# Kernel optimization log

Measured on AMD Instinct MI355X. Metric: run time of the kernel, lower is better.

The kernel has to match this reference:

```python
import jax, jax.numpy as jnp
import numpy as np

N = 50000      # total nodes (50 graphs x 1000 nodes)
G = 50         # number of graphs in the batch
NODE = 1000    # nodes per graph
E = 320000     # total edges (within-graph)
IN = 128
H1, H2 = 64, 128
HEADS = 4
NEG = 0.2      # LeakyReLU negative slope


def setup_inputs() -> dict:
    key = jax.random.key(0)
    ks = jax.random.split(key, 16)
    x = jax.random.normal(ks[0], (N, IN), jnp.float32)
    # edges confined to their own graph: per-graph offsets
    off = (jnp.arange(E) // (E // G)) * NODE
    src = jax.random.randint(ks[1], (E,), 0, NODE) + off
    dst = jax.random.randint(ks[2], (E,), 0, NODE) + off
    node2graph = jnp.arange(N) // NODE

    def lin(k, fan_in, fan_out):
        s = 1.0 / np.sqrt(fan_in)
        kw, kb = jax.random.split(k)
        return (jax.random.uniform(kw, (fan_in, fan_out), jnp.float32, -s, s),
                jax.random.uniform(kb, (fan_out,), jnp.float32, -s, s))

    W_src1, b_src1 = lin(ks[3], IN, HEADS * H1)
    W_dst1, b_dst1 = lin(ks[4], IN, HEADS * H1)
    attn1 = jax.random.normal(ks[5], (HEADS, H1), jnp.float32) * (1.0 / np.sqrt(H1))
    W_src2, b_src2 = lin(ks[6], H1, HEADS * H2)
    W_dst2, b_dst2 = lin(ks[7], H1, HEADS * H2)
    attn2 = jax.random.normal(ks[8], (HEADS, H2), jnp.float32) * (1.0 / np.sqrt(H2))
    gate_w, gate_b = lin(ks[9], H2, 1)
    return dict(x=x, src=src, dst=dst, node2graph=node2graph,
                W_src1=W_src1, b_src1=b_src1, W_dst1=W_dst1, b_dst1=b_dst1, attn1=attn1,
                W_src2=W_src2, b_src2=b_src2, W_dst2=W_dst2, b_dst2=b_dst2, attn2=attn2,
                gate_w=gate_w, gate_b=gate_b)


def gatv2_layer(h, src, dst, W_src, b_src, W_dst, b_dst, attn):
    # DGL GATv2Conv: e_ij = a^T LeakyReLU(W_src h_j + W_dst h_i), edge softmax over dst
    H, D = attn.shape
    fs = (h @ W_src + b_src).reshape(-1, H, D)  # [N,H,D]
    fd = (h @ W_dst + b_dst).reshape(-1, H, D)
    e = jax.nn.leaky_relu(fs[src] + fd[dst], NEG)        # [E,H,D]
    logits = jnp.einsum('ehd,hd->eh', e, attn)           # [E,H]
    m = jax.ops.segment_max(logits, dst, num_segments=h.shape[0])
    ex = jnp.exp(logits - m[dst])
    denom = jax.ops.segment_sum(ex, dst, num_segments=h.shape[0])
    alpha = ex / denom[dst]                              # [E,H]
    out = jax.ops.segment_sum(alpha[:, :, None] * fs[src], dst,
                              num_segments=h.shape[0])   # [N,H,D]
    return out


def reference(x, src, dst, node2graph,
              W_src1, b_src1, W_dst1, b_dst1, attn1,
              W_src2, b_src2, W_dst2, b_dst2, attn2,
              gate_w, gate_b):
    # layer 1 + head-wise maxpool -> [N, H1]
    h = gatv2_layer(x, src, dst, W_src1, b_src1, W_dst1, b_dst1, attn1).max(axis=1)
    # layer 2 + head-wise maxpool -> [N, H2]
    h = gatv2_layer(h, src, dst, W_src2, b_src2, W_dst2, b_dst2, attn2).max(axis=1)
    # global attention pooling: softmax(gate) over nodes per graph, weighted sum
    gate = h @ gate_w + gate_b                           # [N,1]
    gm = jax.ops.segment_max(gate, node2graph, num_segments=G)
    ge = jnp.exp(gate - gm[node2graph])
    gs = jax.ops.segment_sum(ge, node2graph, num_segments=G)
    alpha = ge / gs[node2graph]                          # [N,1]
    return jax.ops.segment_sum(alpha * h, node2graph, num_segments=G)  # [G, H2]
```

## Files before the change

kernel.cpp:

```cpp
#include <hip/hip_runtime.h>
#include <math.h>

#define NN 50000
#define GG 50
#define NODE 1000
#define EE 320000
#define HEADS 4

typedef __attribute__((ext_vector_type(8))) short short8;
typedef __attribute__((ext_vector_type(8))) __bf16 bf16x8;
typedef __attribute__((ext_vector_type(4))) float f32x4;

__device__ __forceinline__ unsigned short f2bf(float f) {
    unsigned int u = __float_as_uint(f);
    u = (u + 0x7fffu + ((u >> 16) & 1u)) >> 16;
    return (unsigned short)u;
}
__device__ __forceinline__ float bf2f(unsigned short s) {
    return __uint_as_float(((unsigned int)s) << 16);
}

__global__ void prep_cvt(const float* __restrict__ x, unsigned short* __restrict__ x_bf,
                         const float* __restrict__ W_src1, const float* __restrict__ W_dst1,
                         unsigned short* __restrict__ Wt1s, unsigned short* __restrict__ Wt1d,
                         const float* __restrict__ W_src2, const float* __restrict__ W_dst2,
                         unsigned short* __restrict__ Wt2s, unsigned short* __restrict__ Wt2d) {
    int i = blockIdx.x * 256 + threadIdx.x;
    int n4 = NN * 128 / 4;
    if (i < n4) {
        float4 f = *(const float4*)(x + (size_t)i * 4);
        ushort4 o;
        o.x = f2bf(f.x); o.y = f2bf(f.y); o.z = f2bf(f.z); o.w = f2bf(f.w);
        *(ushort4*)(x_bf + (size_t)i * 4) = o;
    }
    if (i < 256 * 128) {
        int n = i >> 7, k = i & 127;
        Wt1s[i] = f2bf(W_src1[k * 256 + n]);
        Wt1d[i] = f2bf(W_dst1[k * 256 + n]);
    }
    if (i < 512 * 64) {
        int n = i >> 6, k = i & 63;
        Wt2s[i] = f2bf(W_src2[k * 512 + n]);
        Wt2d[i] = f2bf(W_dst2[k * 512 + n]);
    }
}

__global__ void count_deg(const int* __restrict__ dst, int* __restrict__ deg, int E_) {
    int i = blockIdx.x * 256 + threadIdx.x;
    if (i < E_) atomicAdd(&deg[dst[i]], 1);
}

__global__ void scan1(const int* __restrict__ deg, int* __restrict__ bsum, int Nn) {
    __shared__ int sh[256];
    int i = blockIdx.x * 256 + threadIdx.x;
    sh[threadIdx.x] = (i < Nn) ? deg[i] : 0;
    __syncthreads();
    for (int s = 128; s > 0; s >>= 1) {
        if (threadIdx.x < s) sh[threadIdx.x] += sh[threadIdx.x + s];
        __syncthreads();
    }
    if (threadIdx.x == 0) bsum[blockIdx.x] = sh[0];
}

__global__ void scan3(const int* __restrict__ deg, const int* __restrict__ bsum,
                      int* __restrict__ rowptr, int* __restrict__ cursor, int Nn, int E_) {
    __shared__ int pr[256];
    __shared__ int sh[256];
    int bid = blockIdx.x;
    int pre = 0;
    for (int j = threadIdx.x; j < bid; j += 256) pre += bsum[j];
    pr[threadIdx.x] = pre;
    __syncthreads();
    for (int s = 128; s > 0; s >>= 1) {
        if (threadIdx.x < s) pr[threadIdx.x] += pr[threadIdx.x + s];
        __syncthreads();
    }
    int base = pr[0];
    __syncthreads();
    int i = bid * 256 + threadIdx.x;
    int v = (i < Nn) ? deg[i] : 0;
    sh[threadIdx.x] = v;
    __syncthreads();
    for (int s = 1; s < 256; s <<= 1) {
        int t = (threadIdx.x >= s) ? sh[threadIdx.x - s] : 0;
        __syncthreads();
        sh[threadIdx.x] += t;
        __syncthreads();
    }
    if (i < Nn) {
        int ex = sh[threadIdx.x] - v + base;
        rowptr[i] = ex;
        cursor[i] = ex;
    }
    if (bid == 0 && threadIdx.x == 0) rowptr[Nn] = E_;
}

__global__ void scatter_edges(const int* __restrict__ src, const int* __restrict__ dst,
                              int* __restrict__ cursor, int* __restrict__ csrc, int E_) {
    int i = blockIdx.x * 256 + threadIdx.x;
    if (i < E_) { int pos = atomicAdd(&cursor[dst[i]], 1); csrc[pos] = src[i]; }
}

template<int K>
__global__ __launch_bounds__(256)
void gemm_mfma(const unsigned short* __restrict__ A, const unsigned short* __restrict__ Wt,
               const float* __restrict__ bias, unsigned short* __restrict__ C,
               int M, int Ncols) {
    constexpr int BK = 64;
    __shared__ short A_lds[128 * BK];
    __shared__ short B_lds[128 * BK];
    constexpr int CH = BK / 8;
    constexpr int ROWB = BK * 2;
    int tid = threadIdx.x;
    int lane = tid & 63, wave = tid >> 6;
    int row0 = blockIdx.y * 128, col0 = blockIdx.x * 128;
    int wr = wave >> 1, wc = wave & 1;
    f32x4 acc[4][4] = {};

    for (int k0 = 0; k0 < K; k0 += BK) {
        if (k0) __syncthreads();
        for (int c = tid; c < 128 * CH; c += 256) {
            int r = c / CH, kc = c - r * CH;
            int gr = row0 + r; if (gr >= M) gr = M - 1;
            short8 v = *(const short8*)(A + (size_t)gr * K + k0 + kc * 8);
            *(short8*)((char*)A_lds + r * ROWB + ((kc * 16) ^ ((r & 7) << 4))) = v;
        }
        for (int c = tid; c < 128 * CH; c += 256) {
            int r = c / CH, kc = c - r * CH;
            short8 v = *(const short8*)(Wt + (size_t)(col0 + r) * K + k0 + kc * 8);
            *(short8*)((char*)B_lds + r * ROWB + ((kc * 16) ^ ((r & 7) << 4))) = v;
        }
        __syncthreads();

        #pragma unroll
        for (int ks = 0; ks < BK / 32; ++ks) {
            int kbyte = ks * 64 + ((lane >> 4) << 4);
            short8 a[4], b[4];
            #pragma unroll
            for (int m = 0; m < 4; ++m) {
                int r = wr * 64 + m * 16 + (lane & 15);
                a[m] = *(const short8*)((const char*)A_lds + r * ROWB + (kbyte ^ ((r & 7) << 4)));
            }
            #pragma unroll
            for (int n = 0; n < 4; ++n) {
                int r = wc * 64 + n * 16 + (lane & 15);
                b[n] = *(const short8*)((const char*)B_lds + r * ROWB + (kbyte ^ ((r & 7) << 4)));
            }
            #pragma unroll
            for (int m = 0; m < 4; ++m)
                #pragma unroll
                for (int n = 0; n < 4; ++n)
                    acc[m][n] = __builtin_amdgcn_mfma_f32_16x16x32_bf16(
                        __builtin_bit_cast(bf16x8, a[m]), __builtin_bit_cast(bf16x8, b[n]),
                        acc[m][n], 0, 0, 0);
        }
    }

    #pragma unroll
    for (int m = 0; m < 4; ++m) {
        int grb = row0 + wr * 64 + m * 16 + ((lane >> 4) << 2);
        #pragma unroll
        for (int q = 0; q < 4; ++q) {
            int gr = grb + q;
            if (gr < M) {
                #pragma unroll
                for (int n = 0; n < 4; ++n) {
                    int gc = col0 + wc * 64 + n * 16 + (lane & 15);
                    C[(size_t)gr * Ncols + gc] = f2bf(acc[m][n][q] + bias[gc]);
                }
            }
        }
    }
}

template<int D>
__global__ void gat_fused(const int* __restrict__ rowptr, const int* __restrict__ csrc,
                          const unsigned short* __restrict__ fs, const unsigned short* __restrict__ fd,
                          const float* __restrict__ attn, void* __restrict__ hout, int Nn) {
    int lane = threadIdx.x & 63;
    int wave = (blockIdx.x * blockDim.x + threadIdx.x) >> 6;
    int nw = (gridDim.x * blockDim.x) >> 6;
    constexpr int VE = D / 16;
    constexpr int HD = HEADS * D;
    int head = lane >> 4;
    int doff = (lane & 15) * VE;

    float at[VE];
    #pragma unroll
    for (int j = 0; j < VE; ++j) at[j] = attn[head * D + doff + j];

    for (int n = wave; n < Nn; n += nw) {
        int b = rowptr[n], e_ = rowptr[n + 1];
        float r[VE];
        if (b == e_) {
            #pragma unroll
            for (int k = 0; k < VE; ++k) r[k] = 0.f;
        } else {
            float fdf[VE];
            if constexpr (VE == 4) {
                ushort4 vd = *(const ushort4*)(fd + (size_t)n * HD + lane * 4);
                fdf[0] = bf2f(vd.x); fdf[1] = bf2f(vd.y); fdf[2] = bf2f(vd.z); fdf[3] = bf2f(vd.w);
            } else {
                short8 vd = *(const short8*)(fd + (size_t)n * HD + lane * 8);
                #pragma unroll
                for (int k = 0; k < 8; ++k) fdf[k] = bf2f((unsigned short)vd[k]);
            }
            float m = -INFINITY, l = 0.f;
            float acc[VE];
            #pragma unroll
            for (int k = 0; k < VE; ++k) acc[k] = 0.f;

            for (int j = b; j < e_; ++j) {
                int s = csrc[j];
                float fsf[VE];
                if constexpr (VE == 4) {
                    ushort4 vs = *(const ushort4*)(fs + (size_t)s * HD + lane * 4);
                    fsf[0] = bf2f(vs.x); fsf[1] = bf2f(vs.y); fsf[2] = bf2f(vs.z); fsf[3] = bf2f(vs.w);
                } else {
                    short8 vs = *(const short8*)(fs + (size_t)s * HD + lane * 8);
                    #pragma unroll
                    for (int k = 0; k < 8; ++k) fsf[k] = bf2f((unsigned short)vs[k]);
                }
                float p = 0.f;
                #pragma unroll
                for (int k = 0; k < VE; ++k) {
                    float v = fsf[k] + fdf[k];
                    v = v >= 0.f ? v : 0.2f * v;
                    p += v * at[k];
                }
                p += __shfl_xor(p, 1);
                p += __shfl_xor(p, 2);
                p += __shfl_xor(p, 4);
                p += __shfl_xor(p, 8);
                float mn = fmaxf(m, p);
                float sc = __expf(m - mn);
                float pw = __expf(p - mn);
                l = l * sc + pw;
                #pragma unroll
                for (int k = 0; k < VE; ++k) acc[k] = acc[k] * sc + pw * fsf[k];
                m = mn;
            }
            float inv = 1.f / l;
            #pragma unroll
            for (int k = 0; k < VE; ++k) r[k] = acc[k] * inv;
        }
        #pragma unroll
        for (int k = 0; k < VE; ++k) {
            r[k] = fmaxf(r[k], __shfl_xor(r[k], 16));
            r[k] = fmaxf(r[k], __shfl_xor(r[k], 32));
        }
        if (lane < 16) {
            if constexpr (VE == 4) {
                ushort4 o;
                o.x = f2bf(r[0]); o.y = f2bf(r[1]); o.z = f2bf(r[2]); o.w = f2bf(r[3]);
                *(ushort4*)((unsigned short*)hout + (size_t)n * 64 + doff) = o;
            } else {
                float* hp = (float*)hout + (size_t)n * 128 + doff;
                *(float4*)hp = make_float4(r[0], r[1], r[2], r[3]);
                *(float4*)(hp + 4) = make_float4(r[4], r[5], r[6], r[7]);
            }
        }
    }
}

__global__ void pool_kernel(const float* __restrict__ h2, const float* __restrict__ gate_w,
                            const float* __restrict__ gate_b, float* __restrict__ out) {
    __shared__ float gate[NODE];
    __shared__ float red[256];
    int g = blockIdx.x;
    int tid = threadIdx.x;
    const float* hb = h2 + (size_t)g * NODE * 128;
    float gb = gate_b[0];
    for (int n = tid; n < NODE; n += 256) {
        const float* r = hb + (size_t)n * 128;
        float acc = 0.f;
        #pragma unroll 8
        for (int k = 0; k < 128; ++k) acc += r[k] * gate_w[k];
        gate[n] = acc + gb;
    }
    __syncthreads();
    float m = -INFINITY;
    for (int n = tid; n < NODE; n += 256) m = fmaxf(m, gate[n]);
    red[tid] = m;
    __syncthreads();
    for (int s = 128; s > 0; s >>= 1) {
        if (tid < s) red[tid] = fmaxf(red[tid], red[tid + s]);
        __syncthreads();
    }
    m = red[0];
    __syncthreads();
    float ssum = 0.f;
    for (int n = tid; n < NODE; n += 256) {
        float e = __expf(gate[n] - m);
        gate[n] = e;
        ssum += e;
    }
    red[tid] = ssum;
    __syncthreads();
    for (int s = 128; s > 0; s >>= 1) {
        if (tid < s) red[tid] += red[tid + s];
        __syncthreads();
    }
    float inv = 1.f / red[0];
    __syncthreads();
    float acc = 0.f;
    int half = tid >> 7;
    int k = tid & 127;
    for (int n = half * 500; n < half * 500 + 500; ++n) acc += gate[n] * hb[(size_t)n * 128 + k];
    red[tid] = acc;
    __syncthreads();
    if (tid < 128) out[g * 128 + tid] = (red[tid] + red[tid + 128]) * inv;
}

extern "C" void kernel_launch(void* const* d_in, const int* in_sizes, int n_in,
                              void* d_out, int out_size, void* d_ws, size_t ws_size,
                              hipStream_t stream) {
    const float* x      = (const float*)d_in[0];
    const int*   src    = (const int*)d_in[1];
    const int*   dst    = (const int*)d_in[2];
    const float* W_src1 = (const float*)d_in[4];
    const float* b_src1 = (const float*)d_in[5];
    const float* W_dst1 = (const float*)d_in[6];
    const float* b_dst1 = (const float*)d_in[7];
    const float* attn1  = (const float*)d_in[8];
    const float* W_src2 = (const float*)d_in[9];
    const float* b_src2 = (const float*)d_in[10];
    const float* W_dst2 = (const float*)d_in[11];
    const float* b_dst2 = (const float*)d_in[12];
    const float* attn2  = (const float*)d_in[13];
    const float* gate_w = (const float*)d_in[14];
    const float* gate_b = (const float*)d_in[15];
    float* out = (float*)d_out;

    char* p = (char*)d_ws;
    auto alloc = [&](size_t bytes) -> void* {
        void* r = (void*)p;
        p += (bytes + 255) & ~(size_t)255;
        return r;
    };
    unsigned short* fs     = (unsigned short*)alloc((size_t)NN * 512 * 2);
    unsigned short* fd     = (unsigned short*)alloc((size_t)NN * 512 * 2);
    unsigned short* h1     = (unsigned short*)alloc((size_t)NN * 64 * 2);
    float*          h2     = (float*)alloc((size_t)NN * 128 * 4);
    unsigned short* x_bf   = (unsigned short*)alloc((size_t)NN * 128 * 2);
    unsigned short* Wt1s   = (unsigned short*)alloc((size_t)128 * 256 * 2);
    unsigned short* Wt1d   = (unsigned short*)alloc((size_t)128 * 256 * 2);
    unsigned short* Wt2s   = (unsigned short*)alloc((size_t)64 * 512 * 2);
    unsigned short* Wt2d   = (unsigned short*)alloc((size_t)64 * 512 * 2);
    int*            deg    = (int*)alloc((size_t)NN * 4);
    int*            rowptr = (int*)alloc((size_t)(NN + 1) * 4);
    int*            cursor = (int*)alloc((size_t)NN * 4);
    int*            csrc   = (int*)alloc((size_t)EE * 4);
    int*            bsum   = (int*)alloc(4096);

    prep_cvt<<<(NN * 128 / 4 + 255) / 256, 256, 0, stream>>>(
        x, x_bf, W_src1, W_dst1, Wt1s, Wt1d, W_src2, W_dst2, Wt2s, Wt2d);

    hipMemsetAsync(deg, 0, (size_t)NN * 4, stream);
    count_deg<<<(EE + 255) / 256, 256, 0, stream>>>(dst, deg, EE);
    int nb = (NN + 255) / 256;
    scan1<<<nb, 256, 0, stream>>>(deg, bsum, NN);
    scan3<<<nb, 256, 0, stream>>>(deg, bsum, rowptr, cursor, NN, EE);
    scatter_edges<<<(EE + 255) / 256, 256, 0, stream>>>(src, dst, cursor, csrc, EE);

    int rowtiles = (NN + 127) / 128;

    gemm_mfma<128><<<dim3(2, rowtiles), 256, 0, stream>>>(x_bf, Wt1s, b_src1, fs, NN, 256);
    gemm_mfma<128><<<dim3(2, rowtiles), 256, 0, stream>>>(x_bf, Wt1d, b_dst1, fd, NN, 256);
    gat_fused<64><<<2048, 256, 0, stream>>>(rowptr, csrc, fs, fd, attn1, h1, NN);

    gemm_mfma<64><<<dim3(4, rowtiles), 256, 0, stream>>>(h1, Wt2s, b_src2, fs, NN, 512);
    gemm_mfma<64><<<dim3(4, rowtiles), 256, 0, stream>>>(h1, Wt2d, b_dst2, fd, NN, 512);
    gat_fused<128><<<2048, 256, 0, stream>>>(rowptr, csrc, fs, fd, attn2, h2, NN);

    pool_kernel<<<GG, 256, 0, stream>>>(h2, gate_w, gate_b, out);
}
```

Before: 356.6 us.

## Merge src/dst projections into one GEMM and fuse gate score into GAT

Concatenates the src and dst weight matrices and biases so each layer's projections come from a single GEMM writing an interleaved fs|fd buffer. This halves the reads of the input activations and the launches. Layer-2 aggregation now also computes the per-node gate logit, so the pooling kernel no longer rereads h2 for the dot product. The interleaved layout doubles the row stride for neighbor gathers, which may reduce cache efficiency.

```diff
diff --git a/kernel.cpp b/kernel.cpp
--- a/kernel.cpp
+++ b/kernel.cpp
@@ -22,9 +22,13 @@
 
 __global__ void prep_cvt(const float* __restrict__ x, unsigned short* __restrict__ x_bf,
                          const float* __restrict__ W_src1, const float* __restrict__ W_dst1,
-                         unsigned short* __restrict__ Wt1s, unsigned short* __restrict__ Wt1d,
+                         unsigned short* __restrict__ Wt1cat,
                          const float* __restrict__ W_src2, const float* __restrict__ W_dst2,
-                         unsigned short* __restrict__ Wt2s, unsigned short* __restrict__ Wt2d) {
+                         unsigned short* __restrict__ Wt2cat,
+                         const float* __restrict__ b_src1, const float* __restrict__ b_dst1,
+                         float* __restrict__ bias1cat,
+                         const float* __restrict__ b_src2, const float* __restrict__ b_dst2,
+                         float* __restrict__ bias2cat) {
     int i = blockIdx.x * 256 + threadIdx.x;
     int n4 = NN * 128 / 4;
     if (i < n4) {
@@ -33,16 +37,16 @@
         o.x = f2bf(f.x); o.y = f2bf(f.y); o.z = f2bf(f.z); o.w = f2bf(f.w);
         *(ushort4*)(x_bf + (size_t)i * 4) = o;
     }
-    if (i < 256 * 128) {
+    if (i < 512 * 128) {
         int n = i >> 7, k = i & 127;
-        Wt1s[i] = f2bf(W_src1[k * 256 + n]);
-        Wt1d[i] = f2bf(W_dst1[k * 256 + n]);
-    }
-    if (i < 512 * 64) {
+        Wt1cat[i] = f2bf(n < 256 ? W_src1[k * 256 + n] : W_dst1[k * 256 + (n - 256)]);
+    }
+    if (i < 1024 * 64) {
         int n = i >> 6, k = i & 63;
-        Wt2s[i] = f2bf(W_src2[k * 512 + n]);
-        Wt2d[i] = f2bf(W_dst2[k * 512 + n]);
-    }
+        Wt2cat[i] = f2bf(n < 512 ? W_src2[k * 512 + n] : W_dst2[k * 512 + (n - 512)]);
+    }
+    if (i < 512)  bias1cat[i] = (i < 256) ? b_src1[i] : b_dst1[i - 256];
+    if (i < 1024) bias2cat[i] = (i < 512) ? b_src2[i] : b_dst2[i - 512];
 }
 
 __global__ void count_deg(const int* __restrict__ dst, int* __restrict__ deg, int E_) {
@@ -175,13 +179,16 @@
 
 template<int D>
 __global__ void gat_fused(const int* __restrict__ rowptr, const int* __restrict__ csrc,
-                          const unsigned short* __restrict__ fs, const unsigned short* __restrict__ fd,
-                          const float* __restrict__ attn, void* __restrict__ hout, int Nn) {
+                          const unsigned short* __restrict__ fsfd,
+                          const float* __restrict__ attn, void* __restrict__ hout,
+                          const float* __restrict__ gate_w, const float* __restrict__ gate_b,
+                          float* __restrict__ gate_out, int Nn) {
     int lane = threadIdx.x & 63;
     int wave = (blockIdx.x * blockDim.x + threadIdx.x) >> 6;
     int nw = (gridDim.x * blockDim.x) >> 6;
     constexpr int VE = D / 16;
     constexpr int HD = HEADS * D;
+    constexpr int RS = 2 * HD;
     int head = lane >> 4;
     int doff = (lane & 15) * VE;
 
@@ -198,10 +205,10 @@
         } else {
             float fdf[VE];
             if constexpr (VE == 4) {
-                ushort4 vd = *(const ushort4*)(fd + (size_t)n * HD + lane * 4);
+                ushort4 vd = *(const ushort4*)(fsfd + (size_t)n * RS + HD + lane * 4);
                 fdf[0] = bf2f(vd.x); fdf[1] = bf2f(vd.y); fdf[2] = bf2f(vd.z); fdf[3] = bf2f(vd.w);
             } else {
-                short8 vd = *(const short8*)(fd + (size_t)n * HD + lane * 8);
+                short8 vd = *(const short8*)(fsfd + (size_t)n * RS + HD + lane * 8);
                 #pragma unroll
                 for (int k = 0; k < 8; ++k) fdf[k] = bf2f((unsigned short)vd[k]);
             }
@@ -214,10 +221,10 @@
                 int s = csrc[j];
                 float fsf[VE];
                 if constexpr (VE == 4) {
-                    ushort4 vs = *(const ushort4*)(fs + (size_t)s * HD + lane * 4);
+                    ushort4 vs = *(const ushort4*)(fsfd + (size_t)s * RS + lane * 4);
                     fsf[0] = bf2f(vs.x); fsf[1] = bf2f(vs.y); fsf[2] = bf2f(vs.z); fsf[3] = bf2f(vs.w);
                 } else {
-                    short8 vs = *(const short8*)(fs + (size_t)s * HD + lane * 8);
+                    short8 vs = *(const short8*)(fsfd + (size_t)s * RS + lane * 8);
                     #pragma unroll
                     for (int k = 0; k < 8; ++k) fsf[k] = bf2f((unsigned short)vs[k]);
                 }
@@ -249,6 +256,16 @@
             r[k] = fmaxf(r[k], __shfl_xor(r[k], 16));
             r[k] = fmaxf(r[k], __shfl_xor(r[k], 32));
         }
+        if constexpr (D == 128) {
+            float gp = 0.f;
+            #pragma unroll
+            for (int k = 0; k < VE; ++k) gp += r[k] * gate_w[doff + k];
+            gp += __shfl_xor(gp, 1);
+            gp += __shfl_xor(gp, 2);
+            gp += __shfl_xor(gp, 4);
+            gp += __shfl_xor(gp, 8);
+            if (lane == 0) gate_out[n] = gp + gate_b[0];
+        }
         if (lane < 16) {
             if constexpr (VE == 4) {
                 ushort4 o;
@@ -263,21 +280,14 @@
     }
 }
 
-__global__ void pool_kernel(const float* __restrict__ h2, const float* __restrict__ gate_w,
-                            const float* __restrict__ gate_b, float* __restrict__ out) {
+__global__ void pool_kernel(const float* __restrict__ h2, const float* __restrict__ gatebuf,
+                            float* __restrict__ out) {
     __shared__ float gate[NODE];
     __shared__ float red[256];
     int g = blockIdx.x;
     int tid = threadIdx.x;
     const float* hb = h2 + (size_t)g * NODE * 128;
-    float gb = gate_b[0];
-    for (int n = tid; n < NODE; n += 256) {
-        const float* r = hb + (size_t)n * 128;
-        float acc = 0.f;
-        #pragma unroll 8
-        for (int k = 0; k < 128; ++k) acc += r[k] * gate_w[k];
-        gate[n] = acc + gb;
-    }
+    for (int n = tid; n < NODE; n += 256) gate[n] = gatebuf[g * NODE + n];
     __syncthreads();
     float m = -INFINITY;
     for (int n = tid; n < NODE; n += 256) m = fmaxf(m, gate[n]);
@@ -338,23 +348,24 @@
         p += (bytes + 255) & ~(size_t)255;
         return r;
     };
-    unsigned short* fs     = (unsigned short*)alloc((size_t)NN * 512 * 2);
-    unsigned short* fd     = (unsigned short*)alloc((size_t)NN * 512 * 2);
-    unsigned short* h1     = (unsigned short*)alloc((size_t)NN * 64 * 2);
-    float*          h2     = (float*)alloc((size_t)NN * 128 * 4);
-    unsigned short* x_bf   = (unsigned short*)alloc((size_t)NN * 128 * 2);
-    unsigned short* Wt1s   = (unsigned short*)alloc((size_t)128 * 256 * 2);
-    unsigned short* Wt1d   = (unsigned short*)alloc((size_t)128 * 256 * 2);
-    unsigned short* Wt2s   = (unsigned short*)alloc((size_t)64 * 512 * 2);
-    unsigned short* Wt2d   = (unsigned short*)alloc((size_t)64 * 512 * 2);
-    int*            deg    = (int*)alloc((size_t)NN * 4);
-    int*            rowptr = (int*)alloc((size_t)(NN + 1) * 4);
-    int*            cursor = (int*)alloc((size_t)NN * 4);
-    int*            csrc   = (int*)alloc((size_t)EE * 4);
-    int*            bsum   = (int*)alloc(4096);
+    unsigned short* fsfd    = (unsigned short*)alloc((size_t)NN * 1024 * 2);
+    unsigned short* h1      = (unsigned short*)alloc((size_t)NN * 64 * 2);
+    float*          h2      = (float*)alloc((size_t)NN * 128 * 4);
+    float*          gatebuf = (float*)alloc((size_t)NN * 4);
+    unsigned short* x_bf    = (unsigned short*)alloc((size_t)NN * 128 * 2);
+    unsigned short* Wt1cat  = (unsigned short*)alloc((size_t)512 * 128 * 2);
+    unsigned short* Wt2cat  = (unsigned short*)alloc((size_t)1024 * 64 * 2);
+    float*          bias1   = (float*)alloc(512 * 4);
+    float*          bias2   = (float*)alloc(1024 * 4);
+    int*            deg     = (int*)alloc((size_t)NN * 4);
+    int*            rowptr  = (int*)alloc((size_t)(NN + 1) * 4);
+    int*            cursor  = (int*)alloc((size_t)NN * 4);
+    int*            csrc    = (int*)alloc((size_t)EE * 4);
+    int*            bsum    = (int*)alloc(4096);
 
     prep_cvt<<<(NN * 128 / 4 + 255) / 256, 256, 0, stream>>>(
-        x, x_bf, W_src1, W_dst1, Wt1s, Wt1d, W_src2, W_dst2, Wt2s, Wt2d);
+        x, x_bf, W_src1, W_dst1, Wt1cat, W_src2, W_dst2, Wt2cat,
+        b_src1, b_dst1, bias1, b_src2, b_dst2, bias2);
 
     hipMemsetAsync(deg, 0, (size_t)NN * 4, stream);
     count_deg<<<(EE + 255) / 256, 256, 0, stream>>>(dst, deg, EE);
@@ -365,13 +376,13 @@
 
     int rowtiles = (NN + 127) / 128;
 
-    gemm_mfma<128><<<dim3(2, rowtiles), 256, 0, stream>>>(x_bf, Wt1s, b_src1, fs, NN, 256);
-    gemm_mfma<128><<<dim3(2, rowtiles), 256, 0, stream>>>(x_bf, Wt1d, b_dst1, fd, NN, 256);
-    gat_fused<64><<<2048, 256, 0, stream>>>(rowptr, csrc, fs, fd, attn1, h1, NN);
-
-    gemm_mfma<64><<<dim3(4, rowtiles), 256, 0, stream>>>(h1, Wt2s, b_src2, fs, NN, 512);
-    gemm_mfma<64><<<dim3(4, rowtiles), 256, 0, stream>>>(h1, Wt2d, b_dst2, fd, NN, 512);
-    gat_fused<128><<<2048, 256, 0, stream>>>(rowptr, csrc, fs, fd, attn2, h2, NN);
-
-    pool_kernel<<<GG, 256, 0, stream>>>(h2, gate_w, gate_b, out);
-}
+    gemm_mfma<128><<<dim3(4, rowtiles), 256, 0, stream>>>(x_bf, Wt1cat, bias1, fsfd, NN, 512);
+    gat_fused<64><<<2048, 256, 0, stream>>>(rowptr, csrc, fsfd, attn1, h1,
+                                            nullptr, nullptr, nullptr, NN);
+
+    gemm_mfma<64><<<dim3(8, rowtiles), 256, 0, stream>>>(h1, Wt2cat, bias2, fsfd, NN, 1024);
+    gat_fused<128><<<2048, 256, 0, stream>>>(rowptr, csrc, fsfd, attn2, h2,
+                                             gate_w, gate_b, gatebuf, NN);
+
+    pool_kernel<<<GG, 256, 0, stream>>>(h2, gatebuf, out);
+}
```

Measured after the change: 361.7 us. About the same (+1.4%).
